# Optimization experiments

Measured on AMD Instinct MI355X. Metric: run time of the kernel, lower is better.

## Reference

```python
import jax, jax.numpy as jnp
import numpy as np
from jax import lax

B, S, T, E, H, V = 32, 64, 48, 512, 1024, 32000
PAD = 0


def lstm_cell(x, h, c, W_ih, W_hh, b_ih, b_hh):
    # PyTorch gate order: i, f, g, o
    gates = x @ W_ih.T + b_ih + h @ W_hh.T + b_hh
    i, f, g, o = jnp.split(gates, 4, axis=-1)
    c = jax.nn.sigmoid(f) * c + jax.nn.sigmoid(i) * jnp.tanh(g)
    h = jax.nn.sigmoid(o) * jnp.tanh(c)
    return h, c


def setup_inputs() -> dict:
    key = jax.random.key(0)
    ks = jax.random.split(key, 24)
    sc = 0.02
    n = lambda k, shape: jax.random.normal(k, shape, jnp.float32) * sc
    src_emb = n(ks[0], (V, E)).at[PAD].set(0.0)
    tgt_emb = n(ks[1], (V, E)).at[PAD].set(0.0)
    inp = {
        "input_sequences": jax.random.randint(ks[2], (B, S), 0, V),
        "target_sequences": jax.random.randint(ks[3], (B, T), 0, V),
        "src_emb": src_emb,
        "tgt_emb": tgt_emb,
        "enc_Wih_f": n(ks[4], (4 * H, E)),
        "enc_Whh_f": n(ks[5], (4 * H, H)),
        "enc_bih_f": n(ks[6], (4 * H,)),
        "enc_bhh_f": n(ks[7], (4 * H,)),
        "enc_Wih_b": n(ks[8], (4 * H, E)),
        "enc_Whh_b": n(ks[9], (4 * H, H)),
        "enc_bih_b": n(ks[10], (4 * H,)),
        "enc_bhh_b": n(ks[11], (4 * H,)),
        "dec_Wih": n(ks[12], (4 * H, E + H)),
        "dec_Whh": n(ks[13], (4 * H, H)),
        "dec_bih": n(ks[14], (4 * H,)),
        "dec_bhh": n(ks[15], (4 * H,)),
        "W_init_h": n(ks[16], (H, 2 * H)),
        "W_init_c": n(ks[17], (H, 2 * H)),
        "W_att": n(ks[18], (H, 2 * H)),
        "W_comb": n(ks[19], (H, 3 * H)),
        "W_proj": n(ks[20], (V, H)),
    }
    return inp


def reference(input_sequences, target_sequences, src_emb, tgt_emb,
              enc_Wih_f, enc_Whh_f, enc_bih_f, enc_bhh_f,
              enc_Wih_b, enc_Whh_b, enc_bih_b, enc_bhh_b,
              dec_Wih, dec_Whh, dec_bih, dec_bhh,
              W_init_h, W_init_c, W_att, W_comb, W_proj):
    bsz = input_sequences.shape[0]
    x_src = src_emb[input_sequences.T]  # (S, B, E) time-major

    def make_enc_step(W_ih, W_hh, b_ih, b_hh):
        def step(carry, x):
            h, c = carry
            h, c = lstm_cell(x, h, c, W_ih, W_hh, b_ih, b_hh)
            return (h, c), h
        return step

    h0 = jnp.zeros((bsz, H), x_src.dtype)
    c0 = jnp.zeros((bsz, H), x_src.dtype)
    # bidirectional encoder
    (hf, cf), hs_f = lax.scan(make_enc_step(enc_Wih_f, enc_Whh_f, enc_bih_f, enc_bhh_f), (h0, c0), x_src)
    (hb, cb), hs_b = lax.scan(make_enc_step(enc_Wih_b, enc_Whh_b, enc_bih_b, enc_bhh_b), (h0, c0), x_src[::-1])
    enc_h = jnp.concatenate([hs_f, hs_b[::-1]], axis=-1).transpose(1, 0, 2)  # (B, S, 2H)
    last_hidden = jnp.concatenate([hf, hb], axis=-1)  # (B, 2H)
    last_cell = jnp.concatenate([cf, cb], axis=-1)

    dec_h0 = last_hidden @ W_init_h.T
    dec_c0 = last_cell @ W_init_c.T
    enc_att = enc_h @ W_att.T  # (B, S, H)

    x_tgt = tgt_emb[target_sequences.T]  # (T, B, E)

    def dec_step(carry, e_t):
        h, c, prev_out = carry
        x = jnp.concatenate([e_t, prev_out], axis=-1)  # (B, E+H)
        h, c = lstm_cell(x, h, c, dec_Wih, dec_Whh, dec_bih, dec_bhh)
        scores = jnp.einsum('bh,bsh->bs', h, enc_att)
        attn = jax.nn.softmax(scores, axis=-1)
        ctx = jnp.einsum('bs,bsd->bd', attn, enc_h)  # (B, 2H)
        out = jnp.concatenate([h, ctx], axis=-1) @ W_comb.T  # (B, H)
        return (h, c, out), out

    prev0 = jnp.zeros((bsz, H), x_src.dtype)
    _, outs = lax.scan(dec_step, (dec_h0, dec_c0, prev0), x_tgt)  # (T, B, H)

    logits = outs @ W_proj.T  # (T, B, V)
    P = jax.nn.log_softmax(logits, axis=-1)
    tgt = target_sequences.T  # (T, B)
    # P[t] predicts tgt[t+1]; torch.gather with smaller index truncates P to T-1 steps
    gold = jnp.take_along_axis(P[:-1], tgt[1:][..., None], axis=-1)[..., 0]  # (T-1, B)
    scores = gold.sum(axis=0)  # (B,)
    return scores
```

## Files before the change

### kernel.cpp

```cpp
#include <hip/hip_runtime.h>

typedef short v8s __attribute__((ext_vector_type(8)));
typedef float v4f __attribute__((ext_vector_type(4)));
typedef unsigned short u16;

#define DI __device__ __forceinline__
#define MFMA(a, b, c) __builtin_amdgcn_mfma_f32_16x16x32_bf16(a, b, c, 0, 0, 0)

constexpr int B = 32, S = 64, T = 48, E = 512, H = 1024, V = 32000;
constexpr int TP = T - 1;
constexpr int MROWS = TP * B;
constexpr int NCH = 250;

DI u16 f2bf(float f) {
    unsigned u = __float_as_uint(f);
    unsigned r = (u + 0x7FFFu + ((u >> 16) & 1u)) >> 16;
    return (u16)r;
}
DI float bf2f(u16 h) { return __uint_as_float(((unsigned)h) << 16); }
DI v8s load8(const u16* p) { return *reinterpret_cast<const v8s*>(p); }

typedef __attribute__((address_space(1))) const unsigned int gu32;
typedef __attribute__((address_space(3))) unsigned int lu32;
DI void gload_lds16(const u16* g, u16* l) {
    __builtin_amdgcn_global_load_lds((gu32*)g, (lu32*)l, 16, 0, 0);
}

DI void cstore(unsigned* p, unsigned v) {
    __hip_atomic_store(p, v, __ATOMIC_RELAXED, __HIP_MEMORY_SCOPE_AGENT);
}
DI int cload(const int* p) {
    return __hip_atomic_load(p, __ATOMIC_RELAXED, __HIP_MEMORY_SCOPE_AGENT);
}

DI void gbar2(int* bar, int bid, int nblk, int v) {
    __syncthreads();
    if (bid == 0) {
        int t = threadIdx.x;
        if (t > 0 && t < nblk) {
            while (cload(bar + 16 + t * 4) < v) __builtin_amdgcn_s_sleep(1);
        }
        __syncthreads();
        if (t == 0)
            __hip_atomic_store(bar, v, __ATOMIC_RELAXED, __HIP_MEMORY_SCOPE_AGENT);
    } else {
        if (threadIdx.x == 0) {
            __hip_atomic_store(bar + 16 + bid * 4, v, __ATOMIC_RELAXED,
                               __HIP_MEMORY_SCOPE_AGENT);
            while (cload(bar) < v) __builtin_amdgcn_s_sleep(2);
        }
        __syncthreads();
    }
}

__global__ __launch_bounds__(256) void k_cvt(const float* __restrict__ s,
                                             u16* __restrict__ d, int n4) {
    int i = blockIdx.x * 256 + threadIdx.x;
    if (i >= n4) return;
    float4 v = reinterpret_cast<const float4*>(s)[i];
    ushort4 o;
    o.x = f2bf(v.x); o.y = f2bf(v.y); o.z = f2bf(v.z); o.w = f2bf(v.w);
    reinterpret_cast<ushort4*>(d)[i] = o;
}

__global__ __launch_bounds__(256) void k_embed(const int* __restrict__ seq, int seqstr,
                                               int nsteps, const float* __restrict__ emb,
                                               u16* __restrict__ out) {
    int i = blockIdx.x * 256 + threadIdx.x;
    int total = nsteps * B * (E / 4);
    if (i >= total) return;
    int q = i & 127;
    int sb = i >> 7;
    int b = sb & 31;
    int s = sb >> 5;
    int tok = seq[b * seqstr + s];
    float4 v = reinterpret_cast<const float4*>(emb + (size_t)tok * E)[q];
    ushort4 o;
    o.x = f2bf(v.x); o.y = f2bf(v.y); o.z = f2bf(v.z); o.w = f2bf(v.w);
    reinterpret_cast<ushort4*>(out + ((size_t)(s * B + b)) * E)[q] = o;
}

__global__ __launch_bounds__(256) void k_ench(const u16* __restrict__ hsf,
                                              const u16* __restrict__ hsb,
                                              u16* __restrict__ ench) {
    int id = blockIdx.x * 256 + threadIdx.x;
    int d8 = id & 255; int s = (id >> 8) & 63; int b = id >> 14;
    int d0 = d8 * 8;
    const u16* src = (d0 < H) ? hsf + (((size_t)(s + 1) * B + b)) * H + d0
                              : hsb + (((size_t)(S - s) * B + b)) * H + (d0 - H);
    *reinterpret_cast<v8s*>(ench + ((size_t)b * S + s) * 2 * H + d0) = load8(src);
}

__global__ __launch_bounds__(256) void k_transp(const u16* __restrict__ in,
                                                u16* __restrict__ out, int K, int N) {
    __shared__ u16 t[64][72];
    int nt = blockIdx.x * 64, kt = blockIdx.y * 64;
    int tid = threadIdx.x;
    int r = tid >> 2, cq = (tid & 3) * 16;
    v8s v0 = load8(in + (size_t)(kt + r) * N + nt + cq);
    v8s v1 = load8(in + (size_t)(kt + r) * N + nt + cq + 8);
    #pragma unroll
    for (int e = 0; e < 8; ++e) { t[r][cq + e] = (u16)v0[e]; t[r][cq + 8 + e] = (u16)v1[e]; }
    __syncthreads();
    v8s o0, o1;
    #pragma unroll
    for (int e = 0; e < 8; ++e) { o0[e] = (short)t[cq + e][r]; o1[e] = (short)t[cq + 8 + e][r]; }
    *reinterpret_cast<v8s*>(out + (size_t)(nt + r) * K + kt + cq) = o0;
    *reinterpret_cast<v8s*>(out + (size_t)(nt + r) * K + kt + cq + 8) = o1;
}

__global__ __launch_bounds__(256) void k_tile(const u16* __restrict__ A, int astr,
                                              const u16* __restrict__ W, int wstr,
                                              float* __restrict__ outf,
                                              u16* __restrict__ outb, int ostr,
                                              int ktiles) {
    __shared__ __align__(16) u16 As[128 * 64];
    __shared__ __align__(16) u16 Bs[128 * 64];
    const int tid = threadIdx.x;
    const int lane = tid & 63, wv = tid >> 6;
    const int l15 = lane & 15, lg = lane >> 4;
    const int wr = wv >> 1, wc = wv & 1;
    const int m0 = blockIdx.y * 128, n0 = blockIdx.x * 128;
    const int srow = lane >> 3, sc_ = lane & 7;

    v4f acc[4][4];
    #pragma unroll
    for (int i = 0; i < 4; ++i)
        #pragma unroll
        for (int j = 0; j < 4; ++j) acc[i][j] = v4f{0.f, 0.f, 0.f, 0.f};

    for (int kt = 0; kt < ktiles; ++kt) {
        const int kb = kt * 64;
        #pragma unroll
        for (int i = 0; i < 4; ++i) {
            int chunk = wv * 4 + i;
            int row = chunk * 8 + srow;
            int csw = (sc_ ^ (row & 7)) << 3;
            gload_lds16(A + (size_t)(m0 + row) * astr + kb + csw, As + chunk * 512);
            gload_lds16(W + (size_t)(n0 + row) * wstr + kb + csw, Bs + chunk * 512);
        }
        __syncthreads();
        #pragma unroll
        for (int kk = 0; kk < 2; ++kk) {
            int sw = (((kk << 2) | lg) ^ (l15 & 7)) << 3;
            v8s af[4], bfv[4];
            #pragma unroll
            for (int mi = 0; mi < 4; ++mi)
                af[mi] = load8(As + (wr * 64 + mi * 16 + l15) * 64 + sw);
            #pragma unroll
            for (int ni = 0; ni < 4; ++ni)
                bfv[ni] = load8(Bs + (wc * 64 + ni * 16 + l15) * 64 + sw);
            #pragma unroll
            for (int mi = 0; mi < 4; ++mi)
                #pragma unroll
                for (int ni = 0; ni < 4; ++ni)
                    acc[mi][ni] = MFMA(af[mi], bfv[ni], acc[mi][ni]);
        }
        __syncthreads();
    }
    #pragma unroll
    for (int mi = 0; mi < 4; ++mi)
        #pragma unroll
        for (int rr = 0; rr < 4; ++rr) {
            int row = m0 + wr * 64 + mi * 16 + lg * 4 + rr;
            #pragma unroll
            for (int ni = 0; ni < 4; ++ni) {
                int col = n0 + wc * 64 + ni * 16 + l15;
                if (outf) outf[(size_t)row * ostr + col] = acc[mi][ni][rr];
                else      outb[(size_t)row * ostr + col] = f2bf(acc[mi][ni][rr]);
            }
        }
}

struct Seg { const u16* a; int astr; const u16* w; int wstr; int k; };

__global__ __launch_bounds__(512) void k_mm(Seg s1, Seg s2, float* __restrict__ outf,
                                            u16* __restrict__ outb, int ostr, int ks) {
    const int tid = threadIdx.x;
    const int wv = tid >> 6, lane = tid & 63;
    const int l15 = lane & 15, lg = lane >> 4;
    const int wrow = blockIdx.x * 16 + l15;
    const int k0 = wv * ks, k1 = k0 + ks;
    v4f acc0 = {0.f, 0.f, 0.f, 0.f}, acc1 = {0.f, 0.f, 0.f, 0.f};
    int base = 0;
    auto doseg = [&](const Seg& sg) {
        if (sg.k == 0) return;
        int s0 = k0 > base ? k0 : base;
        int send = base + sg.k;
        int s1e = k1 < send ? k1 : send;
        const u16* wp = sg.w + (size_t)wrow * sg.wstr + 8 * lg;
        const u16* a0p = sg.a + (size_t)l15 * sg.astr + 8 * lg;
        const u16* a1p = sg.a + (size_t)(16 + l15) * sg.astr + 8 * lg;
        #pragma unroll 2
        for (int k = s0; k < s1e; k += 32) {
            int kl = k - base;
            v8s bf = load8(wp + kl);
            v8s af0 = load8(a0p + kl);
            v8s af1 = load8(a1p + kl);
            acc0 = MFMA(af0, bf, acc0);
            acc1 = MFMA(af1, bf, acc1);
        }
        base += sg.k;
    };
    doseg(s1); doseg(s2);

    __shared__ float g[8][32][16];
    #pragma unroll
    for (int r = 0; r < 4; ++r) {
        g[wv][lg * 4 + r][l15] = acc0[r];
        g[wv][16 + lg * 4 + r][l15] = acc1[r];
    }
    __syncthreads();
    {
        int b = tid >> 4, cl = tid & 15;
        float v = 0.f;
        #pragma unroll
        for (int w = 0; w < 8; ++w) v += g[w][b][cl];
        int col = blockIdx.x * 16 + cl;
        if (outb) outb[(size_t)b * ostr + col] = f2bf(v);
        else      outf[(size_t)b * ostr + col] = v;
    }
}

__global__ __launch_bounds__(256) void k_enc(
    const float* __restrict__ xgF, const float* __restrict__ xgB,
    const u16* __restrict__ whhf, const u16* __restrict__ whhb,
    const float* __restrict__ bihF, const float* __restrict__ bhhF,
    const float* __restrict__ bihB, const float* __restrict__ bhhB,
    u16* __restrict__ hsf, u16* __restrict__ hsb,
    float* __restrict__ cfinal, int* __restrict__ bars) {
    const int blk = blockIdx.x;
    const int dir = blk >> 8, bid = blk & 255;
    const int tid = threadIdx.x;
    const u16* whh = dir ? whhb : whhf;
    const float* xg = dir ? xgB : xgF;
    const float* bih = dir ? bihB : bihF;
    const float* bhh = dir ? bhhB : bhhF;
    u16* hs = dir ? hsb : hsf;
    int* bar = bars + dir * 2048;
    const int j0 = bid * 4;
    __shared__ u16 wlds[16 * 1024];
    __shared__ float glds[4][32][16];
    __shared__ u16 htmp[32][4];
    {
        int r = tid >> 4, kc = tid & 15;
        int gate = r >> 2, jl = r & 3;
        const u16* src = whh + (size_t)(gate * H + j0 + jl) * H;
        #pragma unroll
        for (int i = 0; i < 8; ++i) {
            int c = kc + 16 * i;
            v8s v = load8(src + c * 8);
            *reinterpret_cast<v8s*>(wlds + r * 1024 + ((c ^ (r & 7)) * 8)) = v;
        }
    }
    float creg = 0.f;
    const int pb = tid >> 2, pj = tid & 3;
    float bsum[4];
    if (tid < 128) {
        #pragma unroll
        for (int gt = 0; gt < 4; ++gt)
            bsum[gt] = bih[gt * H + j0 + pj] + bhh[gt * H + j0 + pj];
    }
    __syncthreads();
    const int wv = tid >> 6, lane = tid & 63, l15 = lane & 15, lg = lane >> 4;
    for (int s = 0; s < S; ++s) {
        float xv[4];
        if (tid < 128) {
            int xrow = ((dir ? (S - 1 - s) : s) * 32 + pb) * 4096;
            const float* xr = xg + xrow + j0 + pj;
            #pragma unroll
            for (int gt = 0; gt < 4; ++gt) xv[gt] = xr[gt * H];
        }
        const u16* hp = hs + (size_t)s * (B * H);
        const u16* a0 = hp + (size_t)l15 * H + wv * 256 + 8 * lg;
        const u16* a1 = a0 + (size_t)16 * H;
        v4f acc0 = {0.f, 0.f, 0.f, 0.f}, acc1 = {0.f, 0.f, 0.f, 0.f};
        #pragma unroll
        for (int kb = 0; kb < 8; ++kb) {
            int c = wv * 32 + kb * 4 + lg;
            v8s bf = load8(wlds + l15 * 1024 + ((c ^ (l15 & 7)) * 8));
            v8s af0 = load8(a0 + kb * 32);
            v8s af1 = load8(a1 + kb * 32);
            acc0 = MFMA(af0, bf, acc0);
            acc1 = MFMA(af1, bf, acc1);
        }
        #pragma unroll
        for (int r = 0; r < 4; ++r) {
            glds[wv][lg * 4 + r][l15] = acc0[r];
            glds[wv][16 + lg * 4 + r][l15] = acc1[r];
        }
        __syncthreads();
        if (tid < 128) {
            float gv[4];
            #pragma unroll
            for (int gt = 0; gt < 4; ++gt) {
                float v = 0.f;
                #pragma unroll
                for (int w = 0; w < 4; ++w) v += glds[w][pb][gt * 4 + pj];
                gv[gt] = v + xv[gt] + bsum[gt];
            }
            float si = 1.f / (1.f + expf(-gv[0]));
            float sf = 1.f / (1.f + expf(-gv[1]));
            float tg = tanhf(gv[2]);
            float so = 1.f / (1.f + expf(-gv[3]));
            creg = sf * creg + si * tg;
            htmp[pb][pj] = f2bf(so * tanhf(creg));
        }
        __syncthreads();
        if (tid < 64) {
            int rb = tid >> 1, c2 = (tid & 1) * 2;
            unsigned val = (unsigned)htmp[rb][c2] | ((unsigned)htmp[rb][c2 + 1] << 16);
            cstore((unsigned*)(hs + (size_t)(s + 1) * (B * H) + (size_t)rb * H + j0 + c2), val);
        }
        gbar2(bar, bid, 256, s + 1);
    }
    if (tid < 128) cfinal[(size_t)dir * B * H + (size_t)pb * H + j0 + pj] = creg;
}

__global__ __launch_bounds__(512) void k_dec(
    const float* __restrict__ xgD, const u16* __restrict__ dwhh,
    const u16* __restrict__ wfuse, const float* __restrict__ bih,
    const float* __restrict__ bhh, const float* __restrict__ decc,
    const u16* __restrict__ encab, const u16* __restrict__ ench,
    u16* __restrict__ hc, int* __restrict__ bar) {
    const int bid = blockIdx.x, tid = threadIdx.x;
    const int j0 = bid * 4;
    __shared__ u16 wlds[16 * 3072];
    __shared__ float glds[8][32][16];
    __shared__ float hl[1056];
    __shared__ float sc[64], aw[64];
    __shared__ u16 htmp[32][4];
    {
        int r = tid >> 5, kc = tid & 31;
        int gate = r >> 2, jl = r & 3;
        int grow = gate * H + j0 + jl;
        for (int i = 0; i < 12; ++i) {
            int c = kc + 32 * i;
            int k = c * 8;
            v8s wf = load8(wfuse + (size_t)grow * 3072 + k);
            if (k < 1024) {
                v8s wh = load8(dwhh + (size_t)grow * 1024 + k);
                #pragma unroll
                for (int e = 0; e < 8; ++e)
                    wf[e] = (short)f2bf(bf2f((u16)wf[e]) + bf2f((u16)wh[e]));
            }
            *reinterpret_cast<v8s*>(wlds + r * 3072 + ((c ^ (r & 7)) * 8)) = wf;
        }
    }
    const int pb = tid >> 2, pj = tid & 3;
    float creg = 0.f;
    float bsum[4];
    if (tid < 128) {
        creg = decc[(size_t)pb * H + j0 + pj];
        #pragma unroll
        for (int gt = 0; gt < 4; ++gt)
            bsum[gt] = bih[gt * H + j0 + pj] + bhh[gt * H + j0 + pj];
    }
    __syncthreads();
    const int wv = tid >> 6, lane = tid & 63, l15 = lane & 15, lg = lane >> 4;
    const int ab = bid >> 3, ach = bid & 7;
    for (int t = 0; t < T; ++t) {
        const u16* hp = hc + (size_t)t * (B * 3072);
        u16* hn = hc + (size_t)(t + 1) * (B * 3072);
        float xv[4];
        if (tid < 128) {
            const float* xr = xgD + (size_t)(t * 32 + pb) * 4096 + j0 + pj;
            #pragma unroll
            for (int gt = 0; gt < 4; ++gt) xv[gt] = xr[gt * H];
        }
        const u16* a0 = hp + (size_t)l15 * 3072 + wv * 384 + 8 * lg;
        const u16* a1 = a0 + (size_t)16 * 3072;
        v4f acc0 = {0.f, 0.f, 0.f, 0.f}, acc1 = {0.f, 0.f, 0.f, 0.f};
        #pragma unroll
        for (int kb = 0; kb < 12; ++kb) {
            int c = wv * 48 + kb * 4 + lg;
            v8s bf = load8(wlds + l15 * 3072 + ((c ^ (l15 & 7)) * 8));
            v8s af0 = load8(a0 + kb * 32);
            v8s af1 = load8(a1 + kb * 32);
            acc0 = MFMA(af0, bf, acc0);
            acc1 = MFMA(af1, bf, acc1);
        }
        #pragma unroll
        for (int r = 0; r < 4; ++r) {
            glds[wv][lg * 4 + r][l15] = acc0[r];
            glds[wv][16 + lg * 4 + r][l15] = acc1[r];
        }
        __syncthreads();
        if (tid < 128) {
            float gv[4];
            #pragma unroll
            for (int gt = 0; gt < 4; ++gt) {
                float v = 0.f;
                #pragma unroll
                for (int w = 0; w < 8; ++w) v += glds[w][pb][gt * 4 + pj];
                gv[gt] = v + xv[gt] + bsum[gt];
            }
            float si = 1.f / (1.f + expf(-gv[0]));
            float sf = 1.f / (1.f + expf(-gv[1]));
            float tg = tanhf(gv[2]);
            float so = 1.f / (1.f + expf(-gv[3]));
            creg = sf * creg + si * tg;
            htmp[pb][pj] = f2bf(so * tanhf(creg));
        }
        __syncthreads();
        if (tid < 64) {
            int rb = tid >> 1, c2 = (tid & 1) * 2;
            unsigned val = (unsigned)htmp[rb][c2] | ((unsigned)htmp[rb][c2 + 1] << 16);
            cstore((unsigned*)(hn + (size_t)rb * 3072 + j0 + c2), val);
        }
        gbar2(bar, bid, 256, 2 * t + 1);
        {
            const u16* hb = hn + (size_t)ab * 3072;
            for (int i = tid; i < 1024; i += 512)
                hl[((i >> 7) * 132) + (i & 127)] = bf2f(hb[i]);
            __syncthreads();
            {
                int si2 = tid >> 3, pt = tid & 7;
                const u16* ap = encab + ((size_t)(ab * 64 + si2)) * 1024 + pt * 128;
                const float* hq = hl + pt * 132;
                float ps = 0.f;
                #pragma unroll
                for (int x = 0; x < 16; ++x) {
                    v8s v = load8(ap + x * 8);
                    #pragma unroll
                    for (int e = 0; e < 8; ++e) ps += bf2f((u16)v[e]) * hq[x * 8 + e];
                }
                ps += __shfl_xor(ps, 1); ps += __shfl_xor(ps, 2); ps += __shfl_xor(ps, 4);
                if (pt == 0) sc[si2] = ps;
            }
            __syncthreads();
            if (tid < 64) {
                float v = sc[tid];
                float m = v;
                #pragma unroll
                for (int o = 32; o; o >>= 1) m = fmaxf(m, __shfl_xor(m, o));
                float e = expf(v - m), sum = e;
                #pragma unroll
                for (int o = 32; o; o >>= 1) sum += __shfl_xor(sum, o);
                aw[tid] = e / sum;
            }
            __syncthreads();
            if (tid < 128) {
                int d = ach * 256 + tid * 2;
                float c0 = 0.f, c1 = 0.f;
                const u16* ep = ench + (size_t)ab * S * 2048 + d;
                #pragma unroll 8
                for (int s2 = 0; s2 < 64; ++s2) {
                    unsigned uv = *reinterpret_cast<const unsigned*>(ep);
                    float w = aw[s2];
                    c0 += w * bf2f((u16)(uv & 0xFFFF));
                    c1 += w * bf2f((u16)(uv >> 16));
                    ep += 2048;
                }
                unsigned ov = ((unsigned)f2bf(c1) << 16) | f2bf(c0);
                cstore((unsigned*)(hn + (size_t)ab * 3072 + 1024 + d), ov);
            }
        }
        gbar2(bar, bid, 256, 2 * t + 2);
    }
}

__global__ __launch_bounds__(256) void k_sub(float* __restrict__ x,
                                             const float* __restrict__ c) {
    int i = blockIdx.x * 256 + threadIdx.x;
    x[i] -= c[i];
}

__global__ __launch_bounds__(256) void k_hc0(const u16* __restrict__ dech,
                                             u16* __restrict__ hc) {
    int b = blockIdx.x;
    int k = blockIdx.y * 256 + threadIdx.x;
    hc[(size_t)b * 3072 + k] = (k < 1024) ? dech[(size_t)b * 1024 + k] : (u16)0;
}

__global__ __launch_bounds__(512) void k_proj(const u16* __restrict__ A,
                                              const u16* __restrict__ W,
                                              const int* __restrict__ tgt,
                                              float* __restrict__ pmax,
                                              float* __restrict__ psum,
                                              float* __restrict__ pgold) {
    __shared__ __align__(16) u16 As[256 * 64];
    __shared__ __align__(16) u16 Bs[128 * 64];
    __shared__ float red[256][2][3];
    const int tid = threadIdx.x;
    const int lane = tid & 63, wv = tid >> 6;
    const int l15 = lane & 15, lg = lane >> 4;
    const int wr = wv >> 1, wc = wv & 1;
    int orig = blockIdx.x;
    int xcd = orig & 7, loc = orig >> 3;
    int wgid = (xcd < 4 ? xcd * 188 : 752 + (xcd - 4) * 187) + loc;
    int nt = wgid / 6, mt = wgid % 6;
    const int m0 = mt * 256, n0 = nt * 128;
    const int srow = lane >> 3, sc_ = lane & 7;

    v4f acc[4][4];
    #pragma unroll
    for (int i = 0; i < 4; ++i)
        #pragma unroll
        for (int j = 0; j < 4; ++j) acc[i][j] = v4f{0.f, 0.f, 0.f, 0.f};

    for (int kt = 0; kt < 16; ++kt) {
        const int kb = kt * 64;
        #pragma unroll
        for (int i = 0; i < 4; ++i) {
            int chunk = wv * 4 + i;
            int row = chunk * 8 + srow;
            int csw = (sc_ ^ (row & 7)) << 3;
            gload_lds16(A + (size_t)(m0 + row) * 1024 + kb + csw, As + chunk * 512);
        }
        #pragma unroll
        for (int i = 0; i < 2; ++i) {
            int chunk = wv * 2 + i;
            int row = chunk * 8 + srow;
            int csw = (sc_ ^ (row & 7)) << 3;
            gload_lds16(W + (size_t)(n0 + row) * 1024 + kb + csw, Bs + chunk * 512);
        }
        __syncthreads();
        #pragma unroll
        for (int kk = 0; kk < 2; ++kk) {
            int sw = (((kk << 2) | lg) ^ (l15 & 7)) << 3;
            v8s af[4], bfv[4];
            #pragma unroll
            for (int mi = 0; mi < 4; ++mi)
                af[mi] = load8(As + (wr * 64 + mi * 16 + l15) * 64 + sw);
            #pragma unroll
            for (int ni = 0; ni < 4; ++ni)
                bfv[ni] = load8(Bs + (wc * 64 + ni * 16 + l15) * 64 + sw);
            #pragma unroll
            for (int mi = 0; mi < 4; ++mi)
                #pragma unroll
                for (int ni = 0; ni < 4; ++ni)
                    acc[mi][ni] = MFMA(af[mi], bfv[ni], acc[mi][ni]);
        }
        __syncthreads();
    }
    #pragma unroll
    for (int mi = 0; mi < 4; ++mi) {
        #pragma unroll
        for (int rr = 0; rr < 4; ++rr) {
            int lrow = wr * 64 + mi * 16 + lg * 4 + rr;
            int grow = m0 + lrow;
            float vmax = -1e30f;
            #pragma unroll
            for (int ni = 0; ni < 4; ++ni) vmax = fmaxf(vmax, acc[mi][ni][rr]);
            #pragma unroll
            for (int x = 1; x < 16; x <<= 1) vmax = fmaxf(vmax, __shfl_xor(vmax, x));
            float se = 0.f;
            #pragma unroll
            for (int ni = 0; ni < 4; ++ni) se += expf(acc[mi][ni][rr] - vmax);
            #pragma unroll
            for (int x = 1; x < 16; x <<= 1) se += __shfl_xor(se, x);
            int t = grow >> 5, b = grow & 31;
            int g = (grow < MROWS) ? tgt[b * T + t + 1] : -1;
            float gv = 0.f;
            #pragma unroll
            for (int ni = 0; ni < 4; ++ni) {
                int col = n0 + wc * 64 + ni * 16 + l15;
                if (col == g) gv = acc[mi][ni][rr];
            }
            #pragma unroll
            for (int x = 1; x < 16; x <<= 1) gv += __shfl_xor(gv, x);
            if (l15 == 0) {
                red[lrow][wc][0] = vmax;
                red[lrow][wc][1] = se;
                red[lrow][wc][2] = gv;
            }
        }
    }
    __syncthreads();
    if (tid < 256) {
        int grow = m0 + tid;
        if (grow < MROWS) {
            float ma = red[tid][0][0], mb = red[tid][1][0];
            float M = fmaxf(ma, mb);
            float Sv = red[tid][0][1] * expf(ma - M) + red[tid][1][1] * expf(mb - M);
            float G = red[tid][0][2] + red[tid][1][2];
            size_t idx = (size_t)grow * NCH + nt;
            pmax[idx] = M; psum[idx] = Sv; pgold[idx] = G;
        }
    }
}

__global__ __launch_bounds__(256) void k_lse(const float* __restrict__ pmax,
                                             const float* __restrict__ psum,
                                             const float* __restrict__ pgold,
                                             float* __restrict__ logP) {
    int item = blockIdx.x * 4 + (threadIdx.x >> 6);
    int lane = threadIdx.x & 63;
    if (item >= MROWS) return;
    float m = -1e30f, g = 0.f;
    for (int c = lane; c < NCH; c += 64) {
        size_t idx = (size_t)item * NCH + c;
        m = fmaxf(m, pmax[idx]);
        g += pgold[idx];
    }
    for (int o = 32; o; o >>= 1) m = fmaxf(m, __shfl_xor(m, o));
    float s = 0.f;
    for (int c = lane; c < NCH; c += 64) {
        size_t idx = (size_t)item * NCH + c;
        s += psum[idx] * expf(pmax[idx] - m);
    }
    for (int o = 32; o; o >>= 1) { s += __shfl_xor(s, o); g += __shfl_xor(g, o); }
    if (lane == 0) logP[item] = g - (m + logf(s));
}

__global__ __launch_bounds__(64) void k_final(const float* __restrict__ logP,
                                              float* __restrict__ out) {
    int b = threadIdx.x;
    if (b < 32) {
        float s = 0.f;
        for (int t = 0; t < TP; ++t) s += logP[t * 32 + b];
        out[b] = s;
    }
}

extern "C" void kernel_launch(void* const* d_in, const int* in_sizes, int n_in,
                              void* d_out, int out_size, void* d_ws, size_t ws_size,
                              hipStream_t stream) {
    const int*   seq_in  = (const int*)d_in[0];
    const int*   seq_tgt = (const int*)d_in[1];
    const float* src_emb = (const float*)d_in[2];
    const float* tgt_emb = (const float*)d_in[3];
    const float* eWihF = (const float*)d_in[4];
    const float* eWhhF = (const float*)d_in[5];
    const float* eBihF = (const float*)d_in[6];
    const float* eBhhF = (const float*)d_in[7];
    const float* eWihB = (const float*)d_in[8];
    const float* eWhhB = (const float*)d_in[9];
    const float* eBihB = (const float*)d_in[10];
    const float* eBhhB = (const float*)d_in[11];
    const float* dWih  = (const float*)d_in[12];
    const float* dWhh  = (const float*)d_in[13];
    const float* dBih  = (const float*)d_in[14];
    const float* dBhh  = (const float*)d_in[15];
    const float* WinH  = (const float*)d_in[16];
    const float* WinC  = (const float*)d_in[17];
    const float* Watt  = (const float*)d_in[18];
    const float* Wcomb = (const float*)d_in[19];
    const float* Wproj = (const float*)d_in[20];

    char* ws = (char*)d_ws;
    size_t off = 0;
    auto alloc = [&](size_t bytes) -> char* {
        off = (off + 255) & ~(size_t)255;
        char* p = ws + off;
        off += bytes;
        return p;
    };
    const size_t G4 = 4 * (size_t)H;
    const size_t slot = (size_t)B * H;
    u16* wihf = (u16*)alloc(G4 * E * 2);
    u16* whhf = (u16*)alloc(G4 * H * 2);
    u16* wihb = (u16*)alloc(G4 * E * 2);
    u16* whhb = (u16*)alloc(G4 * H * 2);
    u16* dwih = (u16*)alloc(G4 * (E + H) * 2);
    u16* dwhh = (u16*)alloc(G4 * H * 2);
    u16* winh = (u16*)alloc((size_t)H * 2 * H * 2);
    u16* winc = (u16*)alloc((size_t)H * 2 * H * 2);
    u16* watt = (u16*)alloc((size_t)H * 2 * H * 2);
    u16* wcmb = (u16*)alloc((size_t)H * 3 * H * 2);
    u16* wprj = (u16*)alloc((size_t)V * H * 2);
    u16* wcmbT = (u16*)alloc((size_t)3 * H * H * 2);
    u16* wfuse = (u16*)alloc((size_t)G4 * 3 * H * 2);
    u16* xsrc  = (u16*)alloc((size_t)S * B * E * 2);
    u16* xtgt  = (u16*)alloc((size_t)T * B * E * 2);
    u16* hsf   = (u16*)alloc((size_t)(S + 1) * slot * 2);
    u16* hsb   = (u16*)alloc((size_t)(S + 1) * slot * 2);
    u16* ench  = (u16*)alloc((size_t)B * S * 2 * H * 2);
    u16* encab = (u16*)alloc((size_t)B * S * H * 2);
    u16* dech  = (u16*)alloc(slot * 2);
    u16* hc    = (u16*)alloc((size_t)(T + 1) * B * 3072 * 2);
    u16* outsb = (u16*)alloc((size_t)(T * B) * H * 2);
    u16* lcbf  = (u16*)alloc(2 * slot * 2);
    float* xgF  = (float*)alloc((size_t)S * B * G4 * 4);
    float* xgB  = (float*)alloc((size_t)S * B * G4 * 4);
    float* xgD  = (float*)alloc((size_t)T * B * G4 * 4);
    float* cf2  = (float*)alloc(2 * slot * 4);
    float* decc = (float*)alloc(slot * 4);
    float* corr = (float*)alloc((size_t)B * G4 * 4);
    float* pmax  = (float*)alloc((size_t)MROWS * NCH * 4);
    float* psum  = (float*)alloc((size_t)MROWS * NCH * 4);
    float* pgold = (float*)alloc((size_t)MROWS * NCH * 4);
    float* logP  = (float*)alloc((size_t)MROWS * 4);
    int* bars = (int*)alloc(3 * 2048 * 4);
    (void)ws_size; (void)in_sizes; (void)n_in; (void)out_size;

    hipMemsetAsync(hsf, 0, slot * 2, stream);
    hipMemsetAsync(hsb, 0, slot * 2, stream);
    hipMemsetAsync(bars, 0, 3 * 2048 * 4, stream);

    auto cvt = [&](const float* s, u16* d, size_t n) {
        int n4 = (int)(n / 4);
        k_cvt<<<dim3((n4 + 255) / 256), dim3(256), 0, stream>>>(s, d, n4);
    };
    cvt(eWihF, wihf, G4 * E);
    cvt(eWhhF, whhf, G4 * H);
    cvt(eWihB, wihb, G4 * E);
    cvt(eWhhB, whhb, G4 * H);
    cvt(dWih,  dwih, G4 * (E + H));
    cvt(dWhh,  dwhh, G4 * H);
    cvt(WinH,  winh, (size_t)H * 2 * H);
    cvt(WinC,  winc, (size_t)H * 2 * H);
    cvt(Watt,  watt, (size_t)H * 2 * H);
    cvt(Wcomb, wcmb, (size_t)H * 3 * H);
    cvt(Wproj, wprj, (size_t)V * H);

    k_embed<<<dim3((S * B * (E / 4) + 255) / 256), dim3(256), 0, stream>>>(
        seq_in, S, S, src_emb, xsrc);
    k_embed<<<dim3((T * B * (E / 4) + 255) / 256), dim3(256), 0, stream>>>(
        seq_tgt, T, T, tgt_emb, xtgt);

    k_transp<<<dim3(3 * H / 64, H / 64), dim3(256), 0, stream>>>(wcmb, wcmbT, H, 3 * H);

    k_tile<<<dim3(32, 16), dim3(256), 0, stream>>>(xsrc, E, wihf, E, xgF, nullptr, 4096, 8);
    k_tile<<<dim3(32, 16), dim3(256), 0, stream>>>(xsrc, E, wihb, E, xgB, nullptr, 4096, 8);
    k_tile<<<dim3(32, 12), dim3(256), 0, stream>>>(xtgt, E, dwih, E + H, xgD, nullptr, 4096, 8);
    k_tile<<<dim3(24, 32), dim3(256), 0, stream>>>(dwih + E, E + H, wcmbT, H,
                                                   nullptr, wfuse, 3 * H, 16);

    k_enc<<<dim3(512), dim3(256), 0, stream>>>(xgF, xgB, whhf, whhb,
                                               eBihF, eBhhF, eBihB, eBhhB,
                                               hsf, hsb, cf2, bars);

    k_ench<<<dim3(B * S * (2 * H / 8) / 256), dim3(256), 0, stream>>>(hsf, hsb, ench);
    k_tile<<<dim3(8, 16), dim3(256), 0, stream>>>(ench, 2 * H, watt, 2 * H,
                                                  nullptr, encab, H, 32);
    cvt(cf2, lcbf, 2 * slot);

    {
        Seg a1{hsf + (size_t)S * slot, H, winh, 2 * H, H};
        Seg a2{hsb + (size_t)S * slot, H, winh + H, 2 * H, H};
        k_mm<<<dim3(H / 16), dim3(512), 0, stream>>>(a1, a2, nullptr, dech, H, 2 * H / 8);
        Seg c1{lcbf, H, winc, 2 * H, H};
        Seg c2{lcbf + slot, H, winc + H, 2 * H, H};
        k_mm<<<dim3(H / 16), dim3(512), 0, stream>>>(c1, c2, decc, nullptr, H, 2 * H / 8);
        Seg f1{dech, H, wfuse, 3 * H, H};
        Seg f0{nullptr, 0, nullptr, 0, 0};
        k_mm<<<dim3(G4 / 16), dim3(512), 0, stream>>>(f1, f0, corr, nullptr, 4096, H / 8);
        k_sub<<<dim3(B * G4 / 256), dim3(256), 0, stream>>>(xgD, corr);
        k_hc0<<<dim3(B, 12), dim3(256), 0, stream>>>(dech, hc);
    }

    k_dec<<<dim3(256), dim3(512), 0, stream>>>(xgD, dwhh, wfuse, dBih, dBhh, decc,
                                               encab, ench, hc, bars + 4096);

    k_tile<<<dim3(8, 12), dim3(256), 0, stream>>>(hc + B * 3072, 3 * H, wcmb, 3 * H,
                                                  nullptr, outsb, H, 48);

    k_proj<<<dim3(1500), dim3(512), 0, stream>>>(outsb, wprj, seq_tgt, pmax, psum, pgold);
    k_lse<<<dim3((MROWS + 3) / 4), dim3(256), 0, stream>>>(pmax, psum, pgold, logP);
    k_final<<<dim3(1), dim3(64), 0, stream>>>(logP, (float*)d_out);
}
```

Before: 1.543 ms.

## Batch weight conversions, widen encoder blocks, split decoder context reduction

Merges the eleven fp32-to-bf16 weight conversion launches into one multi-segment kernel to cut launch overhead. Doubles the encoder recurrent block to 512 threads (8 waves) so each wave covers half the K range per step, shortening the per-step serial MFMA chain at the cost of a larger cross-wave reduction. Splits the decoder attention context sum over 4 thread groups with a shared-memory partial reduction. Drops the final grid barrier after the last timestep in both recurrent kernels.

Result: faster. 1.420 ms (-8.0%).

```diff
diff --git a/kernel.cpp b/kernel.cpp
--- a/kernel.cpp
+++ b/kernel.cpp
@@ -61,6 +61,26 @@
     ushort4 o;
     o.x = f2bf(v.x); o.y = f2bf(v.y); o.z = f2bf(v.z); o.w = f2bf(v.w);
     reinterpret_cast<ushort4*>(d)[i] = o;
+}
+
+struct CvtD {
+    const float* src[11];
+    u16* dst[11];
+    int n4[11];
+    int start[12];
+};
+__global__ __launch_bounds__(256) void k_cvtm(CvtD d) {
+    int blk = blockIdx.x;
+    int seg = 0;
+    #pragma unroll
+    for (int q = 0; q < 11; ++q)
+        if (blk >= d.start[q + 1]) seg = q + 1;
+    int i = (blk - d.start[seg]) * 256 + threadIdx.x;
+    if (i >= d.n4[seg]) return;
+    float4 v = reinterpret_cast<const float4*>(d.src[seg])[i];
+    ushort4 o;
+    o.x = f2bf(v.x); o.y = f2bf(v.y); o.z = f2bf(v.z); o.w = f2bf(v.w);
+    reinterpret_cast<ushort4*>(d.dst[seg])[i] = o;
 }
 
 __global__ __launch_bounds__(256) void k_embed(const int* __restrict__ seq, int seqstr,
@@ -222,7 +242,7 @@
     }
 }
 
-__global__ __launch_bounds__(256) void k_enc(
+__global__ __launch_bounds__(512) void k_enc(
     const float* __restrict__ xgF, const float* __restrict__ xgB,
     const u16* __restrict__ whhf, const u16* __restrict__ whhb,
     const float* __restrict__ bihF, const float* __restrict__ bhhF,
@@ -240,15 +260,15 @@
     int* bar = bars + dir * 2048;
     const int j0 = bid * 4;
     __shared__ u16 wlds[16 * 1024];
-    __shared__ float glds[4][32][16];
+    __shared__ float glds[8][32][16];
     __shared__ u16 htmp[32][4];
     {
-        int r = tid >> 4, kc = tid & 15;
+        int r = tid >> 5, kc = tid & 31;
         int gate = r >> 2, jl = r & 3;
         const u16* src = whh + (size_t)(gate * H + j0 + jl) * H;
         #pragma unroll
-        for (int i = 0; i < 8; ++i) {
-            int c = kc + 16 * i;
+        for (int i = 0; i < 4; ++i) {
+            int c = kc + 32 * i;
             v8s v = load8(src + c * 8);
             *reinterpret_cast<v8s*>(wlds + r * 1024 + ((c ^ (r & 7)) * 8)) = v;
         }
@@ -272,12 +292,12 @@
             for (int gt = 0; gt < 4; ++gt) xv[gt] = xr[gt * H];
         }
         const u16* hp = hs + (size_t)s * (B * H);
-        const u16* a0 = hp + (size_t)l15 * H + wv * 256 + 8 * lg;
+        const u16* a0 = hp + (size_t)l15 * H + wv * 128 + 8 * lg;
         const u16* a1 = a0 + (size_t)16 * H;
         v4f acc0 = {0.f, 0.f, 0.f, 0.f}, acc1 = {0.f, 0.f, 0.f, 0.f};
         #pragma unroll
-        for (int kb = 0; kb < 8; ++kb) {
-            int c = wv * 32 + kb * 4 + lg;
+        for (int kb = 0; kb < 4; ++kb) {
+            int c = wv * 16 + kb * 4 + lg;
             v8s bf = load8(wlds + l15 * 1024 + ((c ^ (l15 & 7)) * 8));
             v8s af0 = load8(a0 + kb * 32);
             v8s af1 = load8(a1 + kb * 32);
@@ -296,7 +316,7 @@
             for (int gt = 0; gt < 4; ++gt) {
                 float v = 0.f;
                 #pragma unroll
-                for (int w = 0; w < 4; ++w) v += glds[w][pb][gt * 4 + pj];
+                for (int w = 0; w < 8; ++w) v += glds[w][pb][gt * 4 + pj];
                 gv[gt] = v + xv[gt] + bsum[gt];
             }
             float si = 1.f / (1.f + expf(-gv[0]));
@@ -312,7 +332,7 @@
             unsigned val = (unsigned)htmp[rb][c2] | ((unsigned)htmp[rb][c2 + 1] << 16);
             cstore((unsigned*)(hs + (size_t)(s + 1) * (B * H) + (size_t)rb * H + j0 + c2), val);
         }
-        gbar2(bar, bid, 256, s + 1);
+        if (s < S - 1) gbar2(bar, bid, 256, s + 1);
     }
     if (tid < 128) cfinal[(size_t)dir * B * H + (size_t)pb * H + j0 + pj] = creg;
 }
@@ -329,6 +349,7 @@
     __shared__ float glds[8][32][16];
     __shared__ float hl[1056];
     __shared__ float sc[64], aw[64];
+    __shared__ float cpart[4][128][2];
     __shared__ u16 htmp[32][4];
     {
         int r = tid >> 5, kc = tid & 31;
@@ -440,23 +461,33 @@
                 aw[tid] = e / sum;
             }
             __syncthreads();
-            if (tid < 128) {
-                int d = ach * 256 + tid * 2;
+            {
+                int q = tid >> 7, dp = tid & 127;
+                int d = ach * 256 + dp * 2;
+                const u16* ep = ench + (size_t)ab * S * 2048 + (size_t)(q * 16) * 2048 + d;
                 float c0 = 0.f, c1 = 0.f;
-                const u16* ep = ench + (size_t)ab * S * 2048 + d;
                 #pragma unroll 8
-                for (int s2 = 0; s2 < 64; ++s2) {
+                for (int s2 = 0; s2 < 16; ++s2) {
                     unsigned uv = *reinterpret_cast<const unsigned*>(ep);
-                    float w = aw[s2];
+                    float w = aw[q * 16 + s2];
                     c0 += w * bf2f((u16)(uv & 0xFFFF));
                     c1 += w * bf2f((u16)(uv >> 16));
                     ep += 2048;
                 }
+                cpart[q][dp][0] = c0;
+                cpart[q][dp][1] = c1;
+            }
+            __syncthreads();
+            if (tid < 128) {
+                float c0 = cpart[0][tid][0] + cpart[1][tid][0]
+                         + cpart[2][tid][0] + cpart[3][tid][0];
+                float c1 = cpart[0][tid][1] + cpart[1][tid][1]
+                         + cpart[2][tid][1] + cpart[3][tid][1];
                 unsigned ov = ((unsigned)f2bf(c1) << 16) | f2bf(c0);
-                cstore((unsigned*)(hn + (size_t)ab * 3072 + 1024 + d), ov);
-            }
-        }
-        gbar2(bar, bid, 256, 2 * t + 2);
+                cstore((unsigned*)(hn + (size_t)ab * 3072 + 1024 + ach * 256 + tid * 2), ov);
+            }
+        }
+        if (t < T - 1) gbar2(bar, bid, 256, 2 * t + 2);
     }
 }
 
@@ -689,21 +720,26 @@
     hipMemsetAsync(hsb, 0, slot * 2, stream);
     hipMemsetAsync(bars, 0, 3 * 2048 * 4, stream);
 
-    auto cvt = [&](const float* s, u16* d, size_t n) {
-        int n4 = (int)(n / 4);
-        k_cvt<<<dim3((n4 + 255) / 256), dim3(256), 0, stream>>>(s, d, n4);
-    };
-    cvt(eWihF, wihf, G4 * E);
-    cvt(eWhhF, whhf, G4 * H);
-    cvt(eWihB, wihb, G4 * E);
-    cvt(eWhhB, whhb, G4 * H);
-    cvt(dWih,  dwih, G4 * (E + H));
-    cvt(dWhh,  dwhh, G4 * H);
-    cvt(WinH,  winh, (size_t)H * 2 * H);
-    cvt(WinC,  winc, (size_t)H * 2 * H);
-    cvt(Watt,  watt, (size_t)H * 2 * H);
-    cvt(Wcomb, wcmb, (size_t)H * 3 * H);
-    cvt(Wproj, wprj, (size_t)V * H);
+    {
+        CvtD d;
+        const float* srcs[11] = {eWihF, eWhhF, eWihB, eWhhB, dWih, dWhh,
+                                 WinH, WinC, Watt, Wcomb, Wproj};
+        u16* dsts[11] = {wihf, whhf, wihb, whhb, dwih, dwhh,
+                         winh, winc, watt, wcmb, wprj};
+        size_t ns[11] = {G4 * E, G4 * H, G4 * E, G4 * H, G4 * (E + H), G4 * H,
+                         (size_t)H * 2 * H, (size_t)H * 2 * H, (size_t)H * 2 * H,
+                         (size_t)H * 3 * H, (size_t)V * H};
+        int blk = 0;
+        for (int i = 0; i < 11; ++i) {
+            d.src[i] = srcs[i];
+            d.dst[i] = dsts[i];
+            d.n4[i] = (int)(ns[i] / 4);
+            d.start[i] = blk;
+            blk += (d.n4[i] + 255) / 256;
+        }
+        d.start[11] = blk;
+        k_cvtm<<<dim3(blk), dim3(256), 0, stream>>>(d);
+    }
 
     k_embed<<<dim3((S * B * (E / 4) + 255) / 256), dim3(256), 0, stream>>>(
         seq_in, S, S, src_emb, xsrc);
@@ -718,14 +754,17 @@
     k_tile<<<dim3(24, 32), dim3(256), 0, stream>>>(dwih + E, E + H, wcmbT, H,
                                                    nullptr, wfuse, 3 * H, 16);
 
-    k_enc<<<dim3(512), dim3(256), 0, stream>>>(xgF, xgB, whhf, whhb,
+    k_enc<<<dim3(512), dim3(512), 0, stream>>>(xgF, xgB, whhf, whhb,
                                                eBihF, eBhhF, eBihB, eBhhB,
                                                hsf, hsb, cf2, bars);
 
     k_ench<<<dim3(B * S * (2 * H / 8) / 256), dim3(256), 0, stream>>>(hsf, hsb, ench);
     k_tile<<<dim3(8, 16), dim3(256), 0, stream>>>(ench, 2 * H, watt, 2 * H,
                                                   nullptr, encab, H, 32);
-    cvt(cf2, lcbf, 2 * slot);
+    {
+        int n4 = (int)(2 * slot / 4);
+        k_cvt<<<dim3((n4 + 255) / 256), dim3(256), 0, stream>>>(cf2, lcbf, n4);
+    }
 
     {
         Seg a1{hsf + (size_t)S * slot, H, winh, 2 * H, H};
```
